# Performance work log

Measured on AMD Instinct MI355X. Metric: run time of the kernel, lower is better.

The kernel has to match this reference:

```python
import jax, jax.numpy as jnp
import numpy as np

B, S, D, H, FB, K, FC = 16, 512, 256, 8, 128, 64, 32


def setup_inputs() -> dict:
    key = jax.random.key(0)
    ks = jax.random.split(key, 16)
    g = lambda i, shp: jax.random.normal(ks[i], shp, dtype=jnp.float32)
    inp = {
        "B_target": g(0, (B, S, FB)),
        "B_infected": g(1, (B, S, FB)),
        "E_target": g(2, (B, S, D)),
        "E_infected": g(3, (B, S, D)),
        "C_target": jax.random.uniform(ks[4], (B, S, K, FC), dtype=jnp.float32),
        "C_infected": jax.random.uniform(ks[5], (B, S, K, FC), dtype=jnp.float32),
        # learned parameters
        "W_bs": g(6, (FB, 1)) * 0.1,
        "W_cs": g(7, (FC, 1)) * 0.1,
        "W1": g(8, (H, D, D)) * (1.0 / np.sqrt(D)),  # per-head Attn W1, batched
        "W2": g(9, (H, D, D)) * (1.0 / np.sqrt(D)),
        "gamma_bs": jnp.ones((S,), jnp.float32),
        "beta_bs": jnp.zeros((S,), jnp.float32),
        "gamma_cs": jnp.ones((S,), jnp.float32),
        "beta_cs": jnp.zeros((S,), jnp.float32),
        "W_f": g(10, (2, 1)) * 0.1,
    }
    return inp


def _weighted_sum(x, W):
    # tf.nn.softmax over trailing size-1 axis of [F,1] -> all ones (faithful)
    return jnp.squeeze(x @ jax.nn.softmax(W, axis=-1), -1)


def _l2norm(x):
    return x * jax.lax.rsqrt(jnp.maximum(jnp.sum(x * x, -1, keepdims=True), 1e-12))


def _layernorm(x, gamma, beta, eps=1e-16):
    m = jnp.mean(x, -1, keepdims=True)
    v = jnp.mean(jnp.square(x - m), -1, keepdims=True)
    return (x - m) * jax.lax.rsqrt(v + eps) * gamma + beta


def _kld(y_true, y_pred, eps=1e-7):
    yt = jnp.clip(y_true, eps, 1.0)
    yp = jnp.clip(y_pred, eps, 1.0)
    return jnp.sum(yt * jnp.log(yt / yp), -1)


def _attn_br(Bvec, E, W1, W2):
    # batched multi-head version of the per-head Attn loop
    Q = jnp.einsum('bsd,hde->bhse', E, W1)
    Kh = jnp.einsum('bsd,hde->bhse', E, W2)
    scale = 1.0 / jnp.sqrt(jnp.asarray(E.shape[-1], E.dtype))
    scores = jnp.einsum('bhse,bhte->bhst', Q, Kh) * scale  # [b,H,S,S]
    A = jax.nn.softmax(scores, axis=2)  # original softmax(axis=1) on [b,S,S]
    # Dot(axes=(1,1)) of [b,S] with [b,S,S] -> [b,S]; stack heads, transpose -> [b,S,H]
    return jnp.einsum('bs,bhst->bth', Bvec, A)


def reference(B_target, B_infected, E_target, E_infected, C_target, C_infected,
              W_bs, W_cs, W1, W2, gamma_bs, beta_bs, gamma_cs, beta_cs, W_f):
    Bt = _weighted_sum(B_target, W_bs)   # [b,S]
    Bi = _weighted_sum(B_infected, W_bs)
    BR_t = _attn_br(Bt, E_target, W1, W2)    # [b,S,H]
    BR_i = _attn_br(Bi, E_infected, W1, W2)
    # keras CosineSimilarity loss = -cos_sim
    cos = -jnp.sum(_l2norm(BR_i) * _l2norm(BR_t), -1)  # [b,S]
    BS_out = _layernorm(cos, gamma_bs, beta_bs)
    Ct = _weighted_sum(C_target, W_cs)   # [b,S,K]
    Ci = _weighted_sum(C_infected, W_cs)
    Cm = 0.5 * (Ct + Ci)
    Cv = 0.5 * _kld(Ci, Cm) + 0.5 * _kld(Ct, Cm)  # [b,S]
    CS_out = _layernorm(Cv, gamma_cs, beta_cs)
    composite = jnp.stack([BS_out, CS_out], axis=-1)  # [b,S,2]
    out = jnp.squeeze(composite @ jax.nn.softmax(W_f, axis=-1), -1)
    return (out, BS_out, CS_out)
```

## Files before the change

### kernel.cpp

```cpp
#include <hip/hip_runtime.h>

#define NB 16
#define NS 512
#define ND 256
#define NH 8
#define NFB 128
#define NK 64
#define NFC 32

using f16 = _Float16;
using f16x4 = __attribute__((ext_vector_type(4))) f16;
using f16x8 = __attribute__((ext_vector_type(8))) f16;
using f32x4 = __attribute__((ext_vector_type(4))) float;

__device__ inline float waveReduceSum(float v) {
    #pragma unroll
    for (int off = 32; off; off >>= 1) v += __shfl_down(v, off);
    return v;
}

__global__ __launch_bounds__(256) void k_convert(const float* __restrict__ Et, const float* __restrict__ Ei,
                                                 f16* __restrict__ Ot, f16* __restrict__ Oi) {
    const int n4 = NB * NS * ND / 4;
    int i = blockIdx.x * 256 + threadIdx.x;
    const float* src; f16* dst;
    if (i < n4) { src = Et; dst = Ot; }
    else        { src = Ei; dst = Oi; i -= n4; }
    float4 v = ((const float4*)src)[i];
    f16x4 o = { (f16)v.x, (f16)v.y, (f16)v.z, (f16)v.w };
    ((f16x4*)dst)[i] = o;
}

__global__ __launch_bounds__(256) void k_bsum(const float* __restrict__ Bt_in, const float* __restrict__ Bi_in,
                                              float* __restrict__ Bt, float* __restrict__ Bi) {
    int wid = (blockIdx.x * 256 + threadIdx.x) >> 6;
    int lane = threadIdx.x & 63;
    const float* src; float* dst; int row;
    if (wid < NB * NS) { src = Bt_in; dst = Bt; row = wid; }
    else               { src = Bi_in; dst = Bi; row = wid - NB * NS; }
    float2 v = ((const float2*)(src + (size_t)row * NFB))[lane];
    float s = waveReduceSum(v.x + v.y);
    if (lane == 0) dst[row] = s;
}

__global__ __launch_bounds__(256) void k_cv(const float* __restrict__ Ct, const float* __restrict__ Ci,
                                            float* __restrict__ Cv) {
    int gw = (blockIdx.x * 256 + threadIdx.x) >> 6;
    int lane = threadIdx.x & 63;
    const float* pt = Ct + ((size_t)gw * NK + lane) * NFC;
    const float* pi = Ci + ((size_t)gw * NK + lane) * NFC;
    float st = 0.f, si = 0.f;
    #pragma unroll
    for (int j = 0; j < NFC; j += 4) {
        float4 vt = *(const float4*)(pt + j); st += vt.x + vt.y + vt.z + vt.w;
        float4 vi = *(const float4*)(pi + j); si += vi.x + vi.y + vi.z + vi.w;
    }
    float cm = 0.5f * (st + si);
    float yp = fminf(fmaxf(cm, 1e-7f), 1.0f);
    float y1 = fminf(fmaxf(si, 1e-7f), 1.0f);
    float y2 = fminf(fmaxf(st, 1e-7f), 1.0f);
    float term = 0.5f * (y1 * logf(y1 / yp) + y2 * logf(y2 / yp));
    term = waveReduceSum(term);
    if (lane == 0) Cv[gw] = term;
}

__global__ __launch_bounds__(256) void k_mt(const float* __restrict__ W1, const float* __restrict__ W2,
                                            f16* __restrict__ Mth) {
    int h  = blockIdx.x >> 4;
    int j0 = ((blockIdx.x >> 2) & 3) * 64;
    int i0 = (blockIdx.x & 3) * 64;
    const float* A  = W2 + (size_t)h * ND * ND;
    const float* Bm = W1 + (size_t)h * ND * ND;
    __shared__ float Wa[64][36];
    __shared__ float Wb[64][36];
    int tid = threadIdx.x;
    int r = tid >> 4, c = tid & 15;
    float acc[4][4] = {};
    for (int d0 = 0; d0 < ND; d0 += 32) {
        __syncthreads();
        #pragma unroll
        for (int i = 0; i < 2; ++i) {
            int sid = tid + i * 256;
            int row = sid >> 3, seg = sid & 7;
            *(float4*)&Wa[row][seg * 4] = *(const float4*)&A [(size_t)(j0 + row) * ND + d0 + seg * 4];
            *(float4*)&Wb[row][seg * 4] = *(const float4*)&Bm[(size_t)(i0 + row) * ND + d0 + seg * 4];
        }
        __syncthreads();
        #pragma unroll 8
        for (int d = 0; d < 32; ++d) {
            float a0 = Wa[r*4+0][d], a1 = Wa[r*4+1][d], a2 = Wa[r*4+2][d], a3 = Wa[r*4+3][d];
            float b0 = Wb[c*4+0][d], b1 = Wb[c*4+1][d], b2 = Wb[c*4+2][d], b3 = Wb[c*4+3][d];
            acc[0][0] += a0*b0; acc[0][1] += a0*b1; acc[0][2] += a0*b2; acc[0][3] += a0*b3;
            acc[1][0] += a1*b0; acc[1][1] += a1*b1; acc[1][2] += a1*b2; acc[1][3] += a1*b3;
            acc[2][0] += a2*b0; acc[2][1] += a2*b1; acc[2][2] += a2*b2; acc[2][3] += a2*b3;
            acc[3][0] += a3*b0; acc[3][1] += a3*b1; acc[3][2] += a3*b2; acc[3][3] += a3*b3;
        }
    }
    #pragma unroll
    for (int a = 0; a < 4; ++a)
        #pragma unroll
        for (int bb = 0; bb < 4; ++bb)
            Mth[(size_t)h * ND * ND + (size_t)(j0 + r * 4 + a) * ND + (i0 + c * 4 + bb)] = (f16)acc[a][bb];
}

__global__ __launch_bounds__(256) void k_pgemm(const f16* __restrict__ Eft, const f16* __restrict__ Efi,
                                               const f16* __restrict__ Mth,
                                               f16* __restrict__ Pt, f16* __restrict__ Pi) {
    int idx = blockIdx.x;
    const f16* E; f16* P;
    if (idx < 1024) { E = Eft; P = Pt; }
    else            { idx -= 1024; E = Efi; P = Pi; }
    int bh = idx >> 3, b = bh >> 3, h = bh & 7;
    int t = idx & 7;
    int m0 = (t >> 1) * 128, n0 = (t & 1) * 128;
    const f16* A  = E + (size_t)b * NS * ND;
    const f16* Bm = Mth + (size_t)h * ND * ND;
    f16* C = P + (size_t)bh * NS * ND;

    __shared__ f16 As[128 * 40];
    __shared__ f16 Bs[128 * 40];

    int tid = threadIdx.x;
    int lane = tid & 63, w = tid >> 6;
    int wm = (w >> 1) * 64, wn = (w & 1) * 64;
    int l16 = lane & 15, ch = lane >> 4;

    f32x4 acc[4][4] = {};

    for (int k0 = 0; k0 < ND; k0 += 32) {
        __syncthreads();
        #pragma unroll
        for (int i = 0; i < 2; ++i) {
            int sid = tid + i * 256;
            int row = sid >> 2, seg = sid & 3;
            *(int4*)&As[row * 40 + seg * 8] = *(const int4*)&A [(size_t)(m0 + row) * ND + k0 + seg * 8];
            *(int4*)&Bs[row * 40 + seg * 8] = *(const int4*)&Bm[(size_t)(n0 + row) * ND + k0 + seg * 8];
        }
        __syncthreads();
        f16x8 a[4], bb[4];
        #pragma unroll
        for (int mi = 0; mi < 4; ++mi) a[mi]  = *(const f16x8*)&As[(wm + mi * 16 + l16) * 40 + ch * 8];
        #pragma unroll
        for (int ni = 0; ni < 4; ++ni) bb[ni] = *(const f16x8*)&Bs[(wn + ni * 16 + l16) * 40 + ch * 8];
        #pragma unroll
        for (int mi = 0; mi < 4; ++mi)
            #pragma unroll
            for (int ni = 0; ni < 4; ++ni)
                acc[mi][ni] = __builtin_amdgcn_mfma_f32_16x16x32_f16(a[mi], bb[ni], acc[mi][ni], 0, 0, 0);
    }
    #pragma unroll
    for (int mi = 0; mi < 4; ++mi)
        #pragma unroll
        for (int ni = 0; ni < 4; ++ni) {
            int col = n0 + wn + ni * 16 + l16;
            int rbase = m0 + wm + mi * 16 + ch * 4;
            #pragma unroll
            for (int r = 0; r < 4; ++r)
                C[(size_t)(rbase + r) * ND + col] = (f16)acc[mi][ni][r];
        }
}

__global__ __launch_bounds__(256) void k_attn(const f16* __restrict__ Pt, const f16* __restrict__ Pi,
                                              const f16* __restrict__ Eft, const f16* __restrict__ Efi,
                                              const float* __restrict__ Bst, const float* __restrict__ Bsi,
                                              float* __restrict__ BRt, float* __restrict__ BRi) {
    int idx = blockIdx.x;
    const f16 *P, *E; const float* Bvg; float* BR;
    if (idx < 1024) { P = Pt; E = Eft; Bvg = Bst; BR = BRt; }
    else            { idx -= 1024; P = Pi; E = Efi; Bvg = Bsi; BR = BRi; }
    int bh = idx >> 3, b = bh >> 3, h = bh & 7;
    int t0 = (idx & 7) * 64;
    const f16* Pbase = P + (size_t)bh * NS * ND;
    const f16* Ebase = E + (size_t)b * NS * ND;

    __shared__ f16 buf[64 * 264];
    __shared__ float Sc[64][65];
    __shared__ float red[8][64];
    __shared__ float mst[64], lst[64], nst[64];
    __shared__ float Bv[64];

    int tid = threadIdx.x;
    int lane = tid & 63, w = tid >> 6;
    int l16 = lane & 15, ch = lane >> 4;
    int tcol = tid & 63, q = tid >> 6;

    #pragma unroll
    for (int i = 0; i < 8; ++i) {
        int sid = tid + i * 256;
        int row = sid >> 5, seg = sid & 31;
        *(int4*)&buf[row * 264 + seg * 8] = *(const int4*)&Ebase[(size_t)(t0 + row) * ND + seg * 8];
    }
    if (tid < 64) { mst[tid] = -1e30f; lst[tid] = 0.f; nst[tid] = 0.f; }
    __syncthreads();

    f16x8 bfr[4][8];
    #pragma unroll
    for (int ni = 0; ni < 4; ++ni)
        #pragma unroll
        for (int kk = 0; kk < 8; ++kk)
            bfr[ni][kk] = *(const f16x8*)&buf[(ni * 16 + l16) * 264 + kk * 32 + ch * 8];
    __syncthreads();

    for (int s0 = 0; s0 < NS; s0 += 64) {
        #pragma unroll
        for (int i = 0; i < 8; ++i) {
            int sid = tid + i * 256;
            int row = sid >> 5, seg = sid & 31;
            *(int4*)&buf[row * 264 + seg * 8] = *(const int4*)&Pbase[(size_t)(s0 + row) * ND + seg * 8];
        }
        if (tid < 64) Bv[tid] = Bvg[b * NS + s0 + tid];
        __syncthreads();

        f32x4 acc[4] = {};
        #pragma unroll
        for (int kk = 0; kk < 8; ++kk) {
            f16x8 a = *(const f16x8*)&buf[(w * 16 + l16) * 264 + kk * 32 + ch * 8];
            #pragma unroll
            for (int ni = 0; ni < 4; ++ni)
                acc[ni] = __builtin_amdgcn_mfma_f32_16x16x32_f16(a, bfr[ni][kk], acc[ni], 0, 0, 0);
        }
        #pragma unroll
        for (int ni = 0; ni < 4; ++ni)
            #pragma unroll
            for (int r = 0; r < 4; ++r)
                Sc[w * 16 + ch * 4 + r][ni * 16 + l16] = acc[ni][r] * 0.0625f;
        __syncthreads();

        float pm = -1e30f;
        #pragma unroll
        for (int r = 0; r < 16; ++r) pm = fmaxf(pm, Sc[q * 16 + r][tcol]);
        red[q][tcol] = pm;
        __syncthreads();
        if (tid < 64) {
            float tmax = fmaxf(fmaxf(red[0][tid], red[1][tid]), fmaxf(red[2][tid], red[3][tid]));
            float mold = mst[tid];
            float mnew = fmaxf(mold, tmax);
            float alpha = __expf(mold - mnew);
            mst[tid] = mnew; lst[tid] *= alpha; nst[tid] *= alpha;
        }
        __syncthreads();
        float mt = mst[tcol];
        float pe = 0.f, pb = 0.f;
        #pragma unroll
        for (int r = 0; r < 16; ++r) {
            float e = __expf(Sc[q * 16 + r][tcol] - mt);
            pe += e; pb += Bv[q * 16 + r] * e;
        }
        red[q][tcol] = pe; red[q + 4][tcol] = pb;
        __syncthreads();
        if (tid < 64) {
            lst[tid] += red[0][tid] + red[1][tid] + red[2][tid] + red[3][tid];
            nst[tid] += red[4][tid] + red[5][tid] + red[6][tid] + red[7][tid];
        }
        __syncthreads();
    }
    if (tid < 64) BR[((size_t)b * NS + t0 + tid) * NH + h] = nst[tid] / lst[tid];
}

__device__ inline float blockSum512(float v, float* rbuf) {
    v = waveReduceSum(v);
    int lane = threadIdx.x & 63, w = threadIdx.x >> 6;
    __syncthreads();
    if (lane == 0) rbuf[w] = v;
    __syncthreads();
    float s = 0.f;
    #pragma unroll
    for (int i = 0; i < 8; ++i) s += rbuf[i];
    return s;
}

__global__ __launch_bounds__(512) void k_final(const float* __restrict__ BRt, const float* __restrict__ BRi,
                                               const float* __restrict__ Cv,
                                               const float* __restrict__ gbs, const float* __restrict__ bbs,
                                               const float* __restrict__ gcs, const float* __restrict__ bcs,
                                               float* __restrict__ out) {
    __shared__ float rbuf[8];
    int b = blockIdx.x, s = threadIdx.x;
    const float* pt = BRt + ((size_t)b * NS + s) * NH;
    const float* pi = BRi + ((size_t)b * NS + s) * NH;
    float4 t0 = *(const float4*)pt, t1 = *(const float4*)(pt + 4);
    float4 u0 = *(const float4*)pi, u1 = *(const float4*)(pi + 4);
    float dot = t0.x*u0.x + t0.y*u0.y + t0.z*u0.z + t0.w*u0.w
              + t1.x*u1.x + t1.y*u1.y + t1.z*u1.z + t1.w*u1.w;
    float nt  = t0.x*t0.x + t0.y*t0.y + t0.z*t0.z + t0.w*t0.w
              + t1.x*t1.x + t1.y*t1.y + t1.z*t1.z + t1.w*t1.w;
    float nu  = u0.x*u0.x + u0.y*u0.y + u0.z*u0.z + u0.w*u0.w
              + u1.x*u1.x + u1.y*u1.y + u1.z*u1.z + u1.w*u1.w;
    float cosv = -(dot * rsqrtf(fmaxf(nt, 1e-12f)) * rsqrtf(fmaxf(nu, 1e-12f)));

    float mc = blockSum512(cosv, rbuf) * (1.f / 512.f);
    float dc = cosv - mc;
    float vc = blockSum512(dc * dc, rbuf) * (1.f / 512.f);
    float BS = dc * rsqrtf(vc + 1e-16f) * gbs[s] + bbs[s];

    float cv = Cv[(size_t)b * NS + s];
    float mv = blockSum512(cv, rbuf) * (1.f / 512.f);
    float dv = cv - mv;
    float vv = blockSum512(dv * dv, rbuf) * (1.f / 512.f);
    float CS = dv * rsqrtf(vv + 1e-16f) * gcs[s] + bcs[s];

    out[(size_t)b * NS + s] = BS + CS;
    out[(size_t)NB * NS + (size_t)b * NS + s] = BS;
    out[(size_t)2 * NB * NS + (size_t)b * NS + s] = CS;
}

extern "C" void kernel_launch(void* const* d_in, const int* in_sizes, int n_in,
                              void* d_out, int out_size, void* d_ws, size_t ws_size,
                              hipStream_t stream) {
    const float* B_target   = (const float*)d_in[0];
    const float* B_infected = (const float*)d_in[1];
    const float* E_target   = (const float*)d_in[2];
    const float* E_infected = (const float*)d_in[3];
    const float* C_target   = (const float*)d_in[4];
    const float* C_infected = (const float*)d_in[5];
    const float* W1  = (const float*)d_in[8];
    const float* W2  = (const float*)d_in[9];
    const float* gbs = (const float*)d_in[10];
    const float* bbs = (const float*)d_in[11];
    const float* gcs = (const float*)d_in[12];
    const float* bcs = (const float*)d_in[13];
    float* out = (float*)d_out;

    char* ws = (char*)d_ws;
    size_t off = 0;
    auto alloc = [&](size_t n) { char* p = ws + off; off = (off + n + 255) & ~(size_t)255; return p; };
    float* Bt  = (float*)alloc((size_t)NB * NS * 4);
    float* Bi  = (float*)alloc((size_t)NB * NS * 4);
    float* Cv  = (float*)alloc((size_t)NB * NS * 4);
    float* BRt = (float*)alloc((size_t)NB * NS * NH * 4);
    float* BRi = (float*)alloc((size_t)NB * NS * NH * 4);
    f16* Mth = (f16*)alloc((size_t)NH * ND * ND * 2);
    f16* Eft = (f16*)alloc((size_t)NB * NS * ND * 2);
    f16* Efi = (f16*)alloc((size_t)NB * NS * ND * 2);
    f16* Pt  = (f16*)alloc((size_t)NB * NH * NS * ND * 2);
    f16* Pi  = (f16*)alloc((size_t)NB * NH * NS * ND * 2);

    k_convert<<<4096, 256, 0, stream>>>(E_target, E_infected, Eft, Efi);
    k_bsum<<<4096, 256, 0, stream>>>(B_target, B_infected, Bt, Bi);
    k_cv<<<2048, 256, 0, stream>>>(C_target, C_infected, Cv);
    k_mt<<<128, 256, 0, stream>>>(W1, W2, Mth);
    k_pgemm<<<2048, 256, 0, stream>>>(Eft, Efi, Mth, Pt, Pi);
    k_attn<<<2048, 256, 0, stream>>>(Pt, Pi, Eft, Efi, Bt, Bi, BRt, BRi);
    k_final<<<NB, 512, 0, stream>>>(BRt, BRi, Cv, gbs, bbs, gcs, bcs, out);
}
```

Baseline: 351.9 us.

## Fuse projection GEMM and attention-score reduction into one per-(batch,head) kernel

Replaces the separate P = E·M GEMM kernel and the attention kernel with one kernel. Each block of 512 threads handles one (batch, head) pair. It computes 128-row tiles of P into shared memory, multiplies them against E tiles and accumulates the exp-sums and B-weighted sums into shared memory with atomics. This removes the large f16 P intermediate written to and read back from global memory. The softmax no longer subtracts a running max, which simplifies the reduction but risks overflow if scores grow large. The grid drops to 256 large blocks with roughly 130KB of LDS each, so each CU holds one block and latency hiding is reduced.

Result: slower. 366.0 us (+4.0%).

```diff
diff --git a/kernel.cpp b/kernel.cpp
--- a/kernel.cpp
+++ b/kernel.cpp
@@ -17,6 +17,10 @@
     #pragma unroll
     for (int off = 32; off; off >>= 1) v += __shfl_down(v, off);
     return v;
+}
+
+__device__ inline f32x4 mfma16(f16x8 a, f16x8 b, f32x4 c) {
+    return __builtin_amdgcn_mfma_f32_16x16x32_f16(a, b, c, 0, 0, 0);
 }
 
 __global__ __launch_bounds__(256) void k_convert(const float* __restrict__ Et, const float* __restrict__ Ei,
@@ -103,158 +107,105 @@
             Mth[(size_t)h * ND * ND + (size_t)(j0 + r * 4 + a) * ND + (i0 + c * 4 + bb)] = (f16)acc[a][bb];
 }
 
-__global__ __launch_bounds__(256) void k_pgemm(const f16* __restrict__ Eft, const f16* __restrict__ Efi,
-                                               const f16* __restrict__ Mth,
-                                               f16* __restrict__ Pt, f16* __restrict__ Pi) {
-    int idx = blockIdx.x;
-    const f16* E; f16* P;
-    if (idx < 1024) { E = Eft; P = Pt; }
-    else            { idx -= 1024; E = Efi; P = Pi; }
-    int bh = idx >> 3, b = bh >> 3, h = bh & 7;
-    int t = idx & 7;
-    int m0 = (t >> 1) * 128, n0 = (t & 1) * 128;
-    const f16* A  = E + (size_t)b * NS * ND;
-    const f16* Bm = Mth + (size_t)h * ND * ND;
-    f16* C = P + (size_t)bh * NS * ND;
-
-    __shared__ f16 As[128 * 40];
-    __shared__ f16 Bs[128 * 40];
-
-    int tid = threadIdx.x;
-    int lane = tid & 63, w = tid >> 6;
-    int wm = (w >> 1) * 64, wn = (w & 1) * 64;
-    int l16 = lane & 15, ch = lane >> 4;
-
-    f32x4 acc[4][4] = {};
-
-    for (int k0 = 0; k0 < ND; k0 += 32) {
-        __syncthreads();
-        #pragma unroll
-        for (int i = 0; i < 2; ++i) {
-            int sid = tid + i * 256;
-            int row = sid >> 2, seg = sid & 3;
-            *(int4*)&As[row * 40 + seg * 8] = *(const int4*)&A [(size_t)(m0 + row) * ND + k0 + seg * 8];
-            *(int4*)&Bs[row * 40 + seg * 8] = *(const int4*)&Bm[(size_t)(n0 + row) * ND + k0 + seg * 8];
-        }
-        __syncthreads();
-        f16x8 a[4], bb[4];
-        #pragma unroll
-        for (int mi = 0; mi < 4; ++mi) a[mi]  = *(const f16x8*)&As[(wm + mi * 16 + l16) * 40 + ch * 8];
-        #pragma unroll
-        for (int ni = 0; ni < 4; ++ni) bb[ni] = *(const f16x8*)&Bs[(wn + ni * 16 + l16) * 40 + ch * 8];
-        #pragma unroll
-        for (int mi = 0; mi < 4; ++mi)
-            #pragma unroll
-            for (int ni = 0; ni < 4; ++ni)
-                acc[mi][ni] = __builtin_amdgcn_mfma_f32_16x16x32_f16(a[mi], bb[ni], acc[mi][ni], 0, 0, 0);
-    }
-    #pragma unroll
-    for (int mi = 0; mi < 4; ++mi)
-        #pragma unroll
-        for (int ni = 0; ni < 4; ++ni) {
-            int col = n0 + wn + ni * 16 + l16;
-            int rbase = m0 + wm + mi * 16 + ch * 4;
-            #pragma unroll
-            for (int r = 0; r < 4; ++r)
-                C[(size_t)(rbase + r) * ND + col] = (f16)acc[mi][ni][r];
-        }
-}
-
-__global__ __launch_bounds__(256) void k_attn(const f16* __restrict__ Pt, const f16* __restrict__ Pi,
-                                              const f16* __restrict__ Eft, const f16* __restrict__ Efi,
-                                              const float* __restrict__ Bst, const float* __restrict__ Bsi,
-                                              float* __restrict__ BRt, float* __restrict__ BRi) {
-    int idx = blockIdx.x;
-    const f16 *P, *E; const float* Bvg; float* BR;
-    if (idx < 1024) { P = Pt; E = Eft; Bvg = Bst; BR = BRt; }
-    else            { idx -= 1024; P = Pi; E = Efi; Bvg = Bsi; BR = BRi; }
-    int bh = idx >> 3, b = bh >> 3, h = bh & 7;
-    int t0 = (idx & 7) * 64;
-    const f16* Pbase = P + (size_t)bh * NS * ND;
+__global__ __launch_bounds__(512, 1) void k_fused(const f16* __restrict__ Eft, const f16* __restrict__ Efi,
+                                                  const f16* __restrict__ Mth,
+                                                  const float* __restrict__ Bst, const float* __restrict__ Bsi,
+                                                  float* __restrict__ BRt, float* __restrict__ BRi) {
+    int x = blockIdx.x;
+    const f16* E; const float* Bvg; float* BR;
+    if (x < 128) { E = Eft; Bvg = Bst; BR = BRt; }
+    else         { x -= 128; E = Efi; Bvg = Bsi; BR = BRi; }
+    int b = x >> 3, h = x & 7;
     const f16* Ebase = E + (size_t)b * NS * ND;
-
-    __shared__ f16 buf[64 * 264];
-    __shared__ float Sc[64][65];
-    __shared__ float red[8][64];
-    __shared__ float mst[64], lst[64], nst[64];
-    __shared__ float Bv[64];
+    const f16* M = Mth + (size_t)h * ND * ND;
+
+    __shared__ f16 EA[128 * 40];
+    __shared__ f16 Mb[256 * 40];
+    __shared__ f16 Pb[128 * 264];
+    __shared__ f16 Et[64 * 264];
+    __shared__ float pe[NS], pb[NS];
+    __shared__ float Bv[128];
 
     int tid = threadIdx.x;
     int lane = tid & 63, w = tid >> 6;
     int l16 = lane & 15, ch = lane >> 4;
-    int tcol = tid & 63, q = tid >> 6;
-
-    #pragma unroll
-    for (int i = 0; i < 8; ++i) {
-        int sid = tid + i * 256;
-        int row = sid >> 5, seg = sid & 31;
-        *(int4*)&buf[row * 264 + seg * 8] = *(const int4*)&Ebase[(size_t)(t0 + row) * ND + seg * 8];
+
+    pe[tid] = 0.f; pb[tid] = 0.f;
+
+    for (int sb = 0; sb < NS; sb += 128) {
+        f32x4 acc[8][2] = {};
+        for (int k0 = 0; k0 < ND; k0 += 32) {
+            __syncthreads();
+            {
+                int row = tid >> 2, seg = tid & 3;
+                *(int4*)&EA[row * 40 + seg * 8] = *(const int4*)&Ebase[(size_t)(sb + row) * ND + k0 + seg * 8];
+                #pragma unroll
+                for (int i = 0; i < 2; ++i) {
+                    int sid = tid + i * 512;
+                    int r2 = sid >> 2, s2 = sid & 3;
+                    *(int4*)&Mb[r2 * 40 + s2 * 8] = *(const int4*)&M[(size_t)r2 * ND + k0 + s2 * 8];
+                }
+            }
+            __syncthreads();
+            f16x8 b0 = *(const f16x8*)&Mb[(w * 32 +      l16) * 40 + ch * 8];
+            f16x8 b1 = *(const f16x8*)&Mb[(w * 32 + 16 + l16) * 40 + ch * 8];
+            #pragma unroll
+            for (int mt = 0; mt < 8; ++mt) {
+                f16x8 a = *(const f16x8*)&EA[(mt * 16 + l16) * 40 + ch * 8];
+                acc[mt][0] = mfma16(a, b0, acc[mt][0]);
+                acc[mt][1] = mfma16(a, b1, acc[mt][1]);
+            }
+        }
+        #pragma unroll
+        for (int mt = 0; mt < 8; ++mt)
+            #pragma unroll
+            for (int nt = 0; nt < 2; ++nt)
+                #pragma unroll
+                for (int r = 0; r < 4; ++r)
+                    Pb[(mt * 16 + ch * 4 + r) * 264 + w * 32 + nt * 16 + l16] = (f16)acc[mt][nt][r];
+        if (tid < 128) Bv[tid] = Bvg[b * NS + sb + tid];
+
+        for (int t0 = 0; t0 < NS; t0 += 64) {
+            __syncthreads();
+            #pragma unroll
+            for (int i = 0; i < 4; ++i) {
+                int sid = tid + i * 512;
+                int row = sid >> 5, seg = sid & 31;
+                *(int4*)&Et[row * 264 + seg * 8] = *(const int4*)&Ebase[(size_t)(t0 + row) * ND + seg * 8];
+            }
+            __syncthreads();
+            f32x4 sacc[4] = {};
+            #pragma unroll
+            for (int kk = 0; kk < 8; ++kk) {
+                f16x8 a = *(const f16x8*)&Pb[(w * 16 + l16) * 264 + kk * 32 + ch * 8];
+                #pragma unroll
+                for (int nt = 0; nt < 4; ++nt) {
+                    f16x8 bb = *(const f16x8*)&Et[(nt * 16 + l16) * 264 + kk * 32 + ch * 8];
+                    sacc[nt] = mfma16(a, bb, sacc[nt]);
+                }
+            }
+            float bvr[4];
+            #pragma unroll
+            for (int r = 0; r < 4; ++r) bvr[r] = Bv[w * 16 + ch * 4 + r];
+            #pragma unroll
+            for (int nt = 0; nt < 4; ++nt) {
+                float se = 0.f, sw = 0.f;
+                #pragma unroll
+                for (int r = 0; r < 4; ++r) {
+                    float e = __expf(sacc[nt][r] * 0.0625f);
+                    se += e; sw += bvr[r] * e;
+                }
+                se += __shfl_down(se, 32); se += __shfl_down(se, 16);
+                sw += __shfl_down(sw, 32); sw += __shfl_down(sw, 16);
+                if (ch == 0) {
+                    atomicAdd(&pe[t0 + nt * 16 + l16], se);
+                    atomicAdd(&pb[t0 + nt * 16 + l16], sw);
+                }
+            }
+        }
     }
-    if (tid < 64) { mst[tid] = -1e30f; lst[tid] = 0.f; nst[tid] = 0.f; }
     __syncthreads();
-
-    f16x8 bfr[4][8];
-    #pragma unroll
-    for (int ni = 0; ni < 4; ++ni)
-        #pragma unroll
-        for (int kk = 0; kk < 8; ++kk)
-            bfr[ni][kk] = *(const f16x8*)&buf[(ni * 16 + l16) * 264 + kk * 32 + ch * 8];
-    __syncthreads();
-
-    for (int s0 = 0; s0 < NS; s0 += 64) {
-        #pragma unroll
-        for (int i = 0; i < 8; ++i) {
-            int sid = tid + i * 256;
-            int row = sid >> 5, seg = sid & 31;
-            *(int4*)&buf[row * 264 + seg * 8] = *(const int4*)&Pbase[(size_t)(s0 + row) * ND + seg * 8];
-        }
-        if (tid < 64) Bv[tid] = Bvg[b * NS + s0 + tid];
-        __syncthreads();
-
-        f32x4 acc[4] = {};
-        #pragma unroll
-        for (int kk = 0; kk < 8; ++kk) {
-            f16x8 a = *(const f16x8*)&buf[(w * 16 + l16) * 264 + kk * 32 + ch * 8];
-            #pragma unroll
-            for (int ni = 0; ni < 4; ++ni)
-                acc[ni] = __builtin_amdgcn_mfma_f32_16x16x32_f16(a, bfr[ni][kk], acc[ni], 0, 0, 0);
-        }
-        #pragma unroll
-        for (int ni = 0; ni < 4; ++ni)
-            #pragma unroll
-            for (int r = 0; r < 4; ++r)
-                Sc[w * 16 + ch * 4 + r][ni * 16 + l16] = acc[ni][r] * 0.0625f;
-        __syncthreads();
-
-        float pm = -1e30f;
-        #pragma unroll
-        for (int r = 0; r < 16; ++r) pm = fmaxf(pm, Sc[q * 16 + r][tcol]);
-        red[q][tcol] = pm;
-        __syncthreads();
-        if (tid < 64) {
-            float tmax = fmaxf(fmaxf(red[0][tid], red[1][tid]), fmaxf(red[2][tid], red[3][tid]));
-            float mold = mst[tid];
-            float mnew = fmaxf(mold, tmax);
-            float alpha = __expf(mold - mnew);
-            mst[tid] = mnew; lst[tid] *= alpha; nst[tid] *= alpha;
-        }
-        __syncthreads();
-        float mt = mst[tcol];
-        float pe = 0.f, pb = 0.f;
-        #pragma unroll
-        for (int r = 0; r < 16; ++r) {
-            float e = __expf(Sc[q * 16 + r][tcol] - mt);
-            pe += e; pb += Bv[q * 16 + r] * e;
-        }
-        red[q][tcol] = pe; red[q + 4][tcol] = pb;
-        __syncthreads();
-        if (tid < 64) {
-            lst[tid] += red[0][tid] + red[1][tid] + red[2][tid] + red[3][tid];
-            nst[tid] += red[4][tid] + red[5][tid] + red[6][tid] + red[7][tid];
-        }
-        __syncthreads();
-    }
-    if (tid < 64) BR[((size_t)b * NS + t0 + tid) * NH + h] = nst[tid] / lst[tid];
+    BR[((size_t)b * NS + tid) * NH + h] = pb[tid] / pe[tid];
 }
 
 __device__ inline float blockSum512(float v, float* rbuf) {
@@ -332,14 +283,11 @@
     f16* Mth = (f16*)alloc((size_t)NH * ND * ND * 2);
     f16* Eft = (f16*)alloc((size_t)NB * NS * ND * 2);
     f16* Efi = (f16*)alloc((size_t)NB * NS * ND * 2);
-    f16* Pt  = (f16*)alloc((size_t)NB * NH * NS * ND * 2);
-    f16* Pi  = (f16*)alloc((size_t)NB * NH * NS * ND * 2);
 
     k_convert<<<4096, 256, 0, stream>>>(E_target, E_infected, Eft, Efi);
     k_bsum<<<4096, 256, 0, stream>>>(B_target, B_infected, Bt, Bi);
     k_cv<<<2048, 256, 0, stream>>>(C_target, C_infected, Cv);
     k_mt<<<128, 256, 0, stream>>>(W1, W2, Mth);
-    k_pgemm<<<2048, 256, 0, stream>>>(Eft, Efi, Mth, Pt, Pi);
-    k_attn<<<2048, 256, 0, stream>>>(Pt, Pi, Eft, Efi, Bt, Bi, BRt, BRi);
+    k_fused<<<256, 512, 0, stream>>>(Eft, Efi, Mth, Bt, Bi, BRt, BRi);
     k_final<<<NB, 512, 0, stream>>>(BRt, BRi, Cv, gbs, bbs, gcs, bcs, out);
 }
```

## Drop online-softmax max tracking and split attention over query tiles with atomic partial sums

Applied to the files above, without the earlier changes.

Rewrites the attention kernel so each block holds a 128-row tile of P in registers and streams E tiles. It computes exp(score) without subtracting a running max and accumulates column sums of exp and B-weighted exp through shared then global atomics. The final kernel divides these sums per head. This removes the many per-tile syncs and max reductions and the score staging through shared memory. The costs are a memset, float atomics with nondeterministic summation order, and a risk of exp overflow, since no max is subtracted and unbounded scores would break it.

New measurement: 327.1 us. 7.1% less time.

```diff
diff --git a/kernel.cpp b/kernel.cpp
--- a/kernel.cpp
+++ b/kernel.cpp
@@ -17,6 +17,10 @@
     #pragma unroll
     for (int off = 32; off; off >>= 1) v += __shfl_down(v, off);
     return v;
+}
+
+__device__ inline f32x4 mfma16(f16x8 a, f16x8 b, f32x4 c) {
+    return __builtin_amdgcn_mfma_f32_16x16x32_f16(a, b, c, 0, 0, 0);
 }
 
 __global__ __launch_bounds__(256) void k_convert(const float* __restrict__ Et, const float* __restrict__ Ei,
@@ -146,7 +150,7 @@
         for (int mi = 0; mi < 4; ++mi)
             #pragma unroll
             for (int ni = 0; ni < 4; ++ni)
-                acc[mi][ni] = __builtin_amdgcn_mfma_f32_16x16x32_f16(a[mi], bb[ni], acc[mi][ni], 0, 0, 0);
+                acc[mi][ni] = mfma16(a[mi], bb[ni], acc[mi][ni]);
     }
     #pragma unroll
     for (int mi = 0; mi < 4; ++mi)
@@ -160,101 +164,87 @@
         }
 }
 
-__global__ __launch_bounds__(256) void k_attn(const f16* __restrict__ Pt, const f16* __restrict__ Pi,
-                                              const f16* __restrict__ Eft, const f16* __restrict__ Efi,
-                                              const float* __restrict__ Bst, const float* __restrict__ Bsi,
-                                              float* __restrict__ BRt, float* __restrict__ BRi) {
-    int idx = blockIdx.x;
-    const f16 *P, *E; const float* Bvg; float* BR;
-    if (idx < 1024) { P = Pt; E = Eft; Bvg = Bst; BR = BRt; }
-    else            { idx -= 1024; P = Pi; E = Efi; Bvg = Bsi; BR = BRi; }
-    int bh = idx >> 3, b = bh >> 3, h = bh & 7;
-    int t0 = (idx & 7) * 64;
-    const f16* Pbase = P + (size_t)bh * NS * ND;
+__global__ __launch_bounds__(256, 3) void k_attn2(const f16* __restrict__ Pt, const f16* __restrict__ Pi,
+                                                  const f16* __restrict__ Eft, const f16* __restrict__ Efi,
+                                                  const float* __restrict__ Bst, const float* __restrict__ Bsi,
+                                                  float* __restrict__ PEt, float* __restrict__ PBt,
+                                                  float* __restrict__ PEi, float* __restrict__ PBi) {
+    int x = blockIdx.x;
+    const f16 *P, *E; const float* Bvg; float *PE, *PB;
+    if (x < 512) { P = Pt; E = Eft; Bvg = Bst; PE = PEt; PB = PBt; }
+    else         { x -= 512; P = Pi; E = Efi; Bvg = Bsi; PE = PEi; PB = PBi; }
+    int b = x >> 5, h = (x >> 2) & 7, st = x & 3;
+    int s0 = st * 128;
+    const f16* Pbase = P + ((size_t)(b * NH + h) * NS + s0) * ND;
     const f16* Ebase = E + (size_t)b * NS * ND;
-
-    __shared__ f16 buf[64 * 264];
-    __shared__ float Sc[64][65];
-    __shared__ float red[8][64];
-    __shared__ float mst[64], lst[64], nst[64];
-    __shared__ float Bv[64];
+    float* PEo = PE + (size_t)(b * NH + h) * NS;
+    float* PBo = PB + (size_t)(b * NH + h) * NS;
+
+    __shared__ f16 Et[64 * 264];
+    __shared__ float pe_s[NS], pb_s[NS];
 
     int tid = threadIdx.x;
     int lane = tid & 63, w = tid >> 6;
     int l16 = lane & 15, ch = lane >> 4;
-    int tcol = tid & 63, q = tid >> 6;
-
-    #pragma unroll
-    for (int i = 0; i < 8; ++i) {
-        int sid = tid + i * 256;
-        int row = sid >> 5, seg = sid & 31;
-        *(int4*)&buf[row * 264 + seg * 8] = *(const int4*)&Ebase[(size_t)(t0 + row) * ND + seg * 8];
-    }
-    if (tid < 64) { mst[tid] = -1e30f; lst[tid] = 0.f; nst[tid] = 0.f; }
-    __syncthreads();
-
-    f16x8 bfr[4][8];
-    #pragma unroll
-    for (int ni = 0; ni < 4; ++ni)
+
+    pe_s[tid] = 0.f; pe_s[tid + 256] = 0.f;
+    pb_s[tid] = 0.f; pb_s[tid + 256] = 0.f;
+
+    f16x8 af[2][8];
+    #pragma unroll
+    for (int mt = 0; mt < 2; ++mt)
         #pragma unroll
         for (int kk = 0; kk < 8; ++kk)
-            bfr[ni][kk] = *(const f16x8*)&buf[(ni * 16 + l16) * 264 + kk * 32 + ch * 8];
-    __syncthreads();
-
-    for (int s0 = 0; s0 < NS; s0 += 64) {
+            af[mt][kk] = *(const f16x8*)&Pbase[(size_t)(w * 32 + mt * 16 + l16) * ND + kk * 32 + ch * 8];
+
+    float bvr[2][4];
+    #pragma unroll
+    for (int mt = 0; mt < 2; ++mt)
+        #pragma unroll
+        for (int r = 0; r < 4; ++r)
+            bvr[mt][r] = Bvg[b * NS + s0 + w * 32 + mt * 16 + ch * 4 + r];
+
+    for (int t0 = 0; t0 < NS; t0 += 64) {
+        __syncthreads();
         #pragma unroll
         for (int i = 0; i < 8; ++i) {
             int sid = tid + i * 256;
             int row = sid >> 5, seg = sid & 31;
-            *(int4*)&buf[row * 264 + seg * 8] = *(const int4*)&Pbase[(size_t)(s0 + row) * ND + seg * 8];
-        }
-        if (tid < 64) Bv[tid] = Bvg[b * NS + s0 + tid];
-        __syncthreads();
-
-        f32x4 acc[4] = {};
-        #pragma unroll
-        for (int kk = 0; kk < 8; ++kk) {
-            f16x8 a = *(const f16x8*)&buf[(w * 16 + l16) * 264 + kk * 32 + ch * 8];
+            *(int4*)&Et[row * 264 + seg * 8] = *(const int4*)&Ebase[(size_t)(t0 + row) * ND + seg * 8];
+        }
+        __syncthreads();
+        f32x4 sacc[2][4] = {};
+        #pragma unroll
+        for (int kk = 0; kk < 8; ++kk)
             #pragma unroll
-            for (int ni = 0; ni < 4; ++ni)
-                acc[ni] = __builtin_amdgcn_mfma_f32_16x16x32_f16(a, bfr[ni][kk], acc[ni], 0, 0, 0);
-        }
-        #pragma unroll
-        for (int ni = 0; ni < 4; ++ni)
+            for (int nt = 0; nt < 4; ++nt) {
+                f16x8 bf = *(const f16x8*)&Et[(nt * 16 + l16) * 264 + kk * 32 + ch * 8];
+                sacc[0][nt] = mfma16(af[0][kk], bf, sacc[0][nt]);
+                sacc[1][nt] = mfma16(af[1][kk], bf, sacc[1][nt]);
+            }
+        #pragma unroll
+        for (int nt = 0; nt < 4; ++nt) {
+            float se = 0.f, sw = 0.f;
             #pragma unroll
-            for (int r = 0; r < 4; ++r)
-                Sc[w * 16 + ch * 4 + r][ni * 16 + l16] = acc[ni][r] * 0.0625f;
-        __syncthreads();
-
-        float pm = -1e30f;
-        #pragma unroll
-        for (int r = 0; r < 16; ++r) pm = fmaxf(pm, Sc[q * 16 + r][tcol]);
-        red[q][tcol] = pm;
-        __syncthreads();
-        if (tid < 64) {
-            float tmax = fmaxf(fmaxf(red[0][tid], red[1][tid]), fmaxf(red[2][tid], red[3][tid]));
-            float mold = mst[tid];
-            float mnew = fmaxf(mold, tmax);
-            float alpha = __expf(mold - mnew);
-            mst[tid] = mnew; lst[tid] *= alpha; nst[tid] *= alpha;
-        }
-        __syncthreads();
-        float mt = mst[tcol];
-        float pe = 0.f, pb = 0.f;
-        #pragma unroll
-        for (int r = 0; r < 16; ++r) {
-            float e = __expf(Sc[q * 16 + r][tcol] - mt);
-            pe += e; pb += Bv[q * 16 + r] * e;
-        }
-        red[q][tcol] = pe; red[q + 4][tcol] = pb;
-        __syncthreads();
-        if (tid < 64) {
-            lst[tid] += red[0][tid] + red[1][tid] + red[2][tid] + red[3][tid];
-            nst[tid] += red[4][tid] + red[5][tid] + red[6][tid] + red[7][tid];
-        }
-        __syncthreads();
-    }
-    if (tid < 64) BR[((size_t)b * NS + t0 + tid) * NH + h] = nst[tid] / lst[tid];
+            for (int mt = 0; mt < 2; ++mt)
+                #pragma unroll
+                for (int r = 0; r < 4; ++r) {
+                    float e = __expf(sacc[mt][nt][r] * 0.0625f);
+                    se += e; sw += bvr[mt][r] * e;
+                }
+            se += __shfl_down(se, 32); se += __shfl_down(se, 16);
+            sw += __shfl_down(sw, 32); sw += __shfl_down(sw, 16);
+            if (ch == 0) {
+                atomicAdd(&pe_s[t0 + nt * 16 + l16], se);
+                atomicAdd(&pb_s[t0 + nt * 16 + l16], sw);
+            }
+        }
+    }
+    __syncthreads();
+    atomicAdd(&PEo[tid],       pe_s[tid]);
+    atomicAdd(&PEo[tid + 256], pe_s[tid + 256]);
+    atomicAdd(&PBo[tid],       pb_s[tid]);
+    atomicAdd(&PBo[tid + 256], pb_s[tid + 256]);
 }
 
 __device__ inline float blockSum512(float v, float* rbuf) {
@@ -269,23 +259,22 @@
     return s;
 }
 
-__global__ __launch_bounds__(512) void k_final(const float* __restrict__ BRt, const float* __restrict__ BRi,
+__global__ __launch_bounds__(512) void k_final(const float* __restrict__ PEt, const float* __restrict__ PBt,
+                                               const float* __restrict__ PEi, const float* __restrict__ PBi,
                                                const float* __restrict__ Cv,
                                                const float* __restrict__ gbs, const float* __restrict__ bbs,
                                                const float* __restrict__ gcs, const float* __restrict__ bcs,
                                                float* __restrict__ out) {
     __shared__ float rbuf[8];
     int b = blockIdx.x, s = threadIdx.x;
-    const float* pt = BRt + ((size_t)b * NS + s) * NH;
-    const float* pi = BRi + ((size_t)b * NS + s) * NH;
-    float4 t0 = *(const float4*)pt, t1 = *(const float4*)(pt + 4);
-    float4 u0 = *(const float4*)pi, u1 = *(const float4*)(pi + 4);
-    float dot = t0.x*u0.x + t0.y*u0.y + t0.z*u0.z + t0.w*u0.w
-              + t1.x*u1.x + t1.y*u1.y + t1.z*u1.z + t1.w*u1.w;
-    float nt  = t0.x*t0.x + t0.y*t0.y + t0.z*t0.z + t0.w*t0.w
-              + t1.x*t1.x + t1.y*t1.y + t1.z*t1.z + t1.w*t1.w;
-    float nu  = u0.x*u0.x + u0.y*u0.y + u0.z*u0.z + u0.w*u0.w
-              + u1.x*u1.x + u1.y*u1.y + u1.z*u1.z + u1.w*u1.w;
+    float dot = 0.f, nt = 0.f, nu = 0.f;
+    #pragma unroll
+    for (int h = 0; h < NH; ++h) {
+        size_t idx = (size_t)(b * NH + h) * NS + s;
+        float tv = PBt[idx] / PEt[idx];
+        float iv = PBi[idx] / PEi[idx];
+        dot += tv * iv; nt += tv * tv; nu += iv * iv;
+    }
     float cosv = -(dot * rsqrtf(fmaxf(nt, 1e-12f)) * rsqrtf(fmaxf(nu, 1e-12f)));
 
     float mc = blockSum512(cosv, rbuf) * (1.f / 512.f);
@@ -327,19 +316,22 @@
     float* Bt  = (float*)alloc((size_t)NB * NS * 4);
     float* Bi  = (float*)alloc((size_t)NB * NS * 4);
     float* Cv  = (float*)alloc((size_t)NB * NS * 4);
-    float* BRt = (float*)alloc((size_t)NB * NS * NH * 4);
-    float* BRi = (float*)alloc((size_t)NB * NS * NH * 4);
+    float* PEt = (float*)alloc((size_t)NB * NH * NS * 4);
+    float* PBt = (float*)alloc((size_t)NB * NH * NS * 4);
+    float* PEi = (float*)alloc((size_t)NB * NH * NS * 4);
+    float* PBi = (float*)alloc((size_t)NB * NH * NS * 4);
     f16* Mth = (f16*)alloc((size_t)NH * ND * ND * 2);
     f16* Eft = (f16*)alloc((size_t)NB * NS * ND * 2);
     f16* Efi = (f16*)alloc((size_t)NB * NS * ND * 2);
     f16* Pt  = (f16*)alloc((size_t)NB * NH * NS * ND * 2);
     f16* Pi  = (f16*)alloc((size_t)NB * NH * NS * ND * 2);
 
+    hipMemsetAsync(PEt, 0, (size_t)4 * NB * NH * NS * 4, stream);
     k_convert<<<4096, 256, 0, stream>>>(E_target, E_infected, Eft, Efi);
     k_bsum<<<4096, 256, 0, stream>>>(B_target, B_infected, Bt, Bi);
     k_cv<<<2048, 256, 0, stream>>>(C_target, C_infected, Cv);
     k_mt<<<128, 256, 0, stream>>>(W1, W2, Mth);
     k_pgemm<<<2048, 256, 0, stream>>>(Eft, Efi, Mth, Pt, Pi);
-    k_attn<<<2048, 256, 0, stream>>>(Pt, Pi, Eft, Efi, Bt, Bi, BRt, BRi);
-    k_final<<<NB, 512, 0, stream>>>(BRt, BRi, Cv, gbs, bbs, gcs, bcs, out);
-}
+    k_attn2<<<1024, 256, 0, stream>>>(Pt, Pi, Eft, Efi, Bt, Bi, PEt, PBt, PEi, PBi);
+    k_final<<<NB, 512, 0, stream>>>(PEt, PBt, PEi, PBi, Cv, gbs, bbs, gcs, bcs, out);
+}
```
